# Performance work log

Hardware: AMD Instinct MI355X
Metric: run time of the kernel (lower is better)

Reference implementation:

```python
import jax, jax.numpy as jnp
import numpy as np

B, T, C, H = 8, 1024, 768, 12
D = C // H  # head_dim = 64


def setup_inputs() -> dict:
    key = jax.random.key(0)
    ks = jax.random.split(key, 5)
    return {
        "x": jax.random.normal(ks[0], (B, T, C), dtype=jnp.float32),
        "W_in": jax.random.normal(ks[1], (C, 3 * C), dtype=jnp.float32) * 0.02,
        "b_in": jax.random.normal(ks[2], (3 * C,), dtype=jnp.float32) * 0.02,
        "W_out": jax.random.normal(ks[3], (C, C), dtype=jnp.float32) * 0.02,
        "b_out": jax.random.normal(ks[4], (C,), dtype=jnp.float32) * 0.02,
    }


def reference(x, W_in, b_in, W_out, b_out):
    b, t, c = x.shape
    qkv = x @ W_in + b_in                       # [b, t, 3c]
    # NOTE: original code splits as (k, q, v) -- k first!
    k, q, v = jnp.split(qkv, 3, axis=2)
    # [b, h, t, d]
    k = k.reshape(b, t, H, D).transpose(0, 2, 1, 3)
    q = q.reshape(b, t, H, D).transpose(0, 2, 1, 3)
    v = v.reshape(b, t, H, D).transpose(0, 2, 1, 3)
    # NOTE: original applies NO 1/sqrt(d) scaling.
    scores = jnp.einsum("bhqd,bhkd->bhqk", q, k)
    causal = jnp.tril(jnp.ones((t, t), dtype=bool))
    scores = jnp.where(causal[None, None], scores, -jnp.inf)
    attn = jax.nn.softmax(scores, axis=-1)
    y = jnp.einsum("bhqk,bhkd->bhqd", attn, v)  # [b, h, t, d]
    y = y.transpose(0, 2, 1, 3).reshape(b, t, c)
    return y @ W_out + b_out
```

## Files before the change

kernel.cpp:

```cpp
#include <hip/hip_runtime.h>
#include <hip/hip_bf16.h>
#include <stdint.h>


typedef __bf16 bf16;
typedef __attribute__((ext_vector_type(4))) __bf16 bf16x4;
typedef __attribute__((ext_vector_type(8))) __bf16 bf16x8;
typedef __attribute__((ext_vector_type(4))) float f32x4;

#define NB 8
#define NT 1024
#define NC 768
#define NH 12
#define ND 64
#define NM (NB*NT)
#define N3C (3*NC)

typedef __attribute__((address_space(1))) void as1_void;
typedef __attribute__((address_space(3))) void as3_void;

__device__ __forceinline__ void gload_lds16(const void* g, void* l) {
  __builtin_amdgcn_global_load_lds((as1_void*)g, (as3_void*)l, 16, 0, 0);
}


__global__ void k_convert(const float* __restrict__ src, bf16* __restrict__ dst, int n4) {
  int i = blockIdx.x * blockDim.x + threadIdx.x;
  if (i < n4) {
    float4 v = reinterpret_cast<const float4*>(src)[i];
    bf16x4 o = { (bf16)v.x, (bf16)v.y, (bf16)v.z, (bf16)v.w };
    reinterpret_cast<bf16x4*>(dst)[i] = o;
  }
}

__global__ void k_transpose_w(const float* __restrict__ src, bf16* __restrict__ dst,
                              int R, int C) {
  __shared__ float tile[32][33];
  const int c0 = blockIdx.x * 32, r0 = blockIdx.y * 32;
  const int tx = threadIdx.x & 31, ty = threadIdx.x >> 5;
#pragma unroll
  for (int i = 0; i < 4; i++)
    tile[ty + i*8][tx] = src[(size_t)(r0 + ty + i*8) * C + c0 + tx];
  __syncthreads();
#pragma unroll
  for (int i = 0; i < 4; i++)
    dst[(size_t)(c0 + ty + i*8) * R + r0 + tx] = (bf16)tile[tx][ty + i*8];
}

template<int MODE, int TM>
__global__ void __launch_bounds__(256, (TM == 128 ? 3 : 4))
k_gemm_bt(const bf16* __restrict__ A, const bf16* __restrict__ Bt,
          const float* __restrict__ bias, float* __restrict__ Cout,
          bf16* __restrict__ qp, bf16* __restrict__ kp,
          bf16* __restrict__ vp,
          int M, int N, int K) {
  constexpr int ACH = TM / 64;
  constexpr int MF  = TM / 32;
  constexpr int WM  = TM / 2;
  __shared__ __align__(16) bf16 As[3][TM*32];
  __shared__ __align__(16) bf16 Bs[3][128*32];
  const int tm = blockIdx.x * TM, tn = blockIdx.y * 128;
  const int tid = threadIdx.x, lane = tid & 63, w = tid >> 6;
  const int wr = w >> 1, wc = w & 1;
  const int lr = lane & 15, lhi = lane >> 4;
  const int srow = tid >> 2;
  const int scol = ((tid & 3) ^ ((tid >> 3) & 3)) * 8;
  const int cswz = (lhi ^ ((lr >> 1) & 3)) * 16;
  const int nk = K / 32;

  auto stage = [&](bf16* as, bf16* bs, int kt) {
#pragma unroll
    for (int ch = 0; ch < ACH; ch++)
      gload_lds16(A + (size_t)(tm + ch*64 + srow) * K + kt + scol,
                  (char*)as + ch*4096 + tid*16);
#pragma unroll
    for (int ch = 0; ch < 2; ch++)
      gload_lds16(Bt + (size_t)(tn + ch*64 + srow) * K + kt + scol,
                  (char*)bs + ch*4096 + tid*16);
  };

  f32x4 acc[MF][4];
#pragma unroll
  for (int m = 0; m < MF; m++)
#pragma unroll
    for (int n = 0; n < 4; n++) acc[m][n] = (f32x4){0.f, 0.f, 0.f, 0.f};

  bf16 *a0 = As[0], *a1 = As[1], *a2 = As[2];
  bf16 *b0 = Bs[0], *b1 = Bs[1], *b2 = Bs[2];
  stage(a0, b0, 0);
  stage(a1, b1, 32);

  for (int t = 0; t < nk; ++t) {
    const int ktn = (t + 2 < nk ? t + 2 : nk - 1) * 32;
    stage(a2, b2, ktn);
    if constexpr (ACH == 2) asm volatile("s_waitcnt vmcnt(8)" ::: "memory");
    else                    asm volatile("s_waitcnt vmcnt(6)" ::: "memory");
    __builtin_amdgcn_s_barrier();

    bf16x8 af[MF], bfr[4];
#pragma unroll
    for (int m = 0; m < MF; m++)
      af[m] = *reinterpret_cast<const bf16x8*>(
          (const char*)a0 + (wr*WM + m*16 + lr) * 64 + cswz);
#pragma unroll
    for (int n = 0; n < 4; n++)
      bfr[n] = *reinterpret_cast<const bf16x8*>(
          (const char*)b0 + (wc*64 + n*16 + lr) * 64 + cswz);
#pragma unroll
    for (int m = 0; m < MF; m++)
#pragma unroll
      for (int n = 0; n < 4; n++)
        acc[m][n] = __builtin_amdgcn_mfma_f32_16x16x32_bf16(af[m], bfr[n], acc[m][n], 0, 0, 0);

    __builtin_amdgcn_s_barrier();

    bf16* ra = a0; a0 = a1; a1 = a2; a2 = ra;
    bf16* rb = b0; b0 = b1; b1 = b2; b2 = rb;
  }
  asm volatile("s_waitcnt vmcnt(0)" ::: "memory");

  if (MODE == 0) {
#pragma unroll
    for (int m = 0; m < MF; m++)
#pragma unroll
      for (int n = 0; n < 4; n++) {
        const int col = tn + wc*64 + n*16 + lr;
        const float bv = bias[col];
#pragma unroll
        for (int j = 0; j < 4; j++) {
          const int row = tm + wr*WM + m*16 + lhi*4 + j;
          Cout[(size_t)row * N + col] = acc[m][n][j] + bv;
        }
      }
  } else {
    const int part = tn / NC;
#pragma unroll
    for (int m = 0; m < MF; m++)
#pragma unroll
      for (int n = 0; n < 4; n++) {
        const int col = tn + wc*64 + n*16 + lr;
        const float bv = bias[col];
        const int cp = col - part * NC;
        const int h = cp >> 6, d = cp & 63;
#pragma unroll
        for (int j = 0; j < 4; j++) {
          const int row = tm + wr*WM + m*16 + lhi*4 + j;
          const int b0i = row >> 10, t = row & 1023;
          const int bh = b0i * NH + h;
          const bf16 val = (bf16)(acc[m][n][j] + bv);
          if (part == 2) {
            const size_t idx =
                ((((size_t)bh*16 + (t>>6))*4 + (d>>4))*2 + ((t>>5)&1))*512
                + (size_t)((d&15) + ((t>>3)&3)*16)*8 + (t&7);
            vp[idx] = val;
          } else {
            const size_t idx =
                (((size_t)bh*64 + (t>>4))*2 + (d>>5))*512
                + (size_t)(((d>>3)&3)*16 + (t&15))*8 + (d&7);
            if (part == 0) kp[idx] = val; else qp[idx] = val;
          }
        }
      }
  }
}

__global__ void __launch_bounds__(64, 2)
k_attn(const bf16* __restrict__ qpack, const bf16* __restrict__ kpack,
       const bf16* __restrict__ vpack, bf16* __restrict__ y) {
  const int bh = blockIdx.x, b = bh / NH, h = bh % NH;
  const int p = blockIdx.y;
  const int lane = threadIdx.x;
  const int lr = lane & 15, lhi = lane >> 4;
  __shared__ __align__(16) bf16 P[32][68];

#define LOAD_K(DST, K0)                                                        \
  {                                                                            \
    _Pragma("unroll")                                                          \
    for (int g = 0; g < 4; g++)                                                \
      _Pragma("unroll")                                                        \
      for (int h2 = 0; h2 < 2; h2++)                                           \
        DST[g][h2] = *reinterpret_cast<const bf16x8*>(                         \
            kpack + (((size_t)bh*64 + ((K0)>>4) + g)*2 + h2)*512 + lane*8);    \
  }

#define ATTN_STEP(KCUR, KNXT, KB)                                              \
  {                                                                            \
    const int k0 = (KB) * 64;                                                  \
    const int kn = ((KB) + 1 < nkb) ? k0 + 64 : k0;                            \
                        \
    bf16x8 vf[4][2];                                                           \
    _Pragma("unroll")                                                          \
    for (int dg = 0; dg < 4; dg++)                                             \
      _Pragma("unroll")                                                        \
      for (int kk = 0; kk < 2; kk++)                                           \
        vf[dg][kk] = *reinterpret_cast<const bf16x8*>(                         \
            vpack + ((((size_t)bh*16 + (k0>>6))*4 + dg)*2 + kk)*512 + lane*8); \
                   \
    LOAD_K(KNXT, kn);                                                          \
    f32x4 S[2][4];                                                             \
    _Pragma("unroll")                                                          \
    for (int m = 0; m < 2; m++)                                                \
      _Pragma("unroll")                                                        \
      for (int g = 0; g < 4; g++) S[m][g] = (f32x4){0.f, 0.f, 0.f, 0.f};       \
    _Pragma("unroll")                                                          \
    for (int g = 0; g < 4; g++)                                                \
      _Pragma("unroll")                                                        \
      for (int m = 0; m < 2; m++) {                                            \
        S[m][g] = __builtin_amdgcn_mfma_f32_16x16x32_bf16(qf[m][0], KCUR[g][0],\
                                                          S[m][g], 0, 0, 0);   \
        S[m][g] = __builtin_amdgcn_mfma_f32_16x16x32_bf16(qf[m][1], KCUR[g][1],\
                                                          S[m][g], 0, 0, 0);   \
      }                                                                        \
    const bool need_mask = ((KB) == nkb - 1);                                  \
    _Pragma("unroll")                                                          \
    for (int m = 0; m < 2; m++)                                                \
      _Pragma("unroll")                                                        \
      for (int g = 0; g < 4; g++) {                                            \
        const int key = k0 + g*16 + lr;                                        \
        _Pragma("unroll")                                                      \
        for (int j = 0; j < 4; j++) {                                          \
          float s = S[m][g][j];                                                \
          if (need_mask) {                                                     \
            const int row = qbase + m*16 + lhi*4 + j;                          \
            if (key > row) s = -1e30f;                                         \
          }                                                                    \
          const float ppv = __expf(s);   \
          L[m][j] += ppv;                                                      \
          P[m*16 + lhi*4 + j][g*16 + lr] = (bf16)ppv;                          \
        }                                                                      \
      }                                                                        \
    _Pragma("unroll")                                                          \
    for (int m = 0; m < 2; m++)                                                \
      _Pragma("unroll")                                                        \
      for (int kk = 0; kk < 2; kk++) {                                         \
        bf16x8 pf = *reinterpret_cast<const bf16x8*>(&P[m*16 + lr][kk*32 + lhi*8]); \
        _Pragma("unroll")                                                      \
        for (int dg = 0; dg < 4; dg++)                                         \
          O[m][dg] = __builtin_amdgcn_mfma_f32_16x16x32_bf16(pf, vf[dg][kk],   \
                                                             O[m][dg], 0, 0, 0); \
      }                                                                        \
  }

#pragma unroll 1
  for (int half = 0; half < 2; half++) {
    const int qt = half ? (31 - p) : p;
    const int qbase = qt * 32;
    const int nkb = (qbase >> 6) + 1;

    bf16x8 qf[2][2];
#pragma unroll
    for (int m = 0; m < 2; m++)
#pragma unroll
      for (int kk = 0; kk < 2; kk++)
        qf[m][kk] = *reinterpret_cast<const bf16x8*>(
            qpack + (((size_t)bh*64 + (qbase>>4) + m)*2 + kk)*512 + lane*8);

    f32x4 O[2][4];
    float L[2][4];
#pragma unroll
    for (int m = 0; m < 2; m++) {
#pragma unroll
      for (int d = 0; d < 4; d++) O[m][d] = (f32x4){0.f, 0.f, 0.f, 0.f};
#pragma unroll
      for (int j = 0; j < 4; j++) L[m][j] = 0.f;
    }

    bf16x8 kfA[4][2], kfB[4][2];
    LOAD_K(kfA, 0);
    int kb = 0;
#pragma unroll 1
    while (true) {
      ATTN_STEP(kfA, kfB, kb);
      kb++;
      if (kb >= nkb) break;
      ATTN_STEP(kfB, kfA, kb);
      kb++;
      if (kb >= nkb) break;
    }

#pragma unroll
    for (int m = 0; m < 2; m++)
#pragma unroll
      for (int j = 0; j < 4; j++) {
        float l = L[m][j];
        l += __shfl_xor(l, 1);
        l += __shfl_xor(l, 2);
        l += __shfl_xor(l, 4);
        l += __shfl_xor(l, 8);
        L[m][j] = 1.0f / l;
      }

#pragma unroll
    for (int m = 0; m < 2; m++)
#pragma unroll
      for (int dg = 0; dg < 4; dg++)
#pragma unroll
        for (int j = 0; j < 4; j++) {
          const int row = qbase + m*16 + lhi*4 + j;
          const int col = h*ND + dg*16 + lr;
          y[(size_t)(b*NT + row) * NC + col] = (bf16)(O[m][dg][j] * L[m][j]);
        }
  }
#undef ATTN_STEP
#undef LOAD_K
}

extern "C" void kernel_launch(void* const* d_in, const int* in_sizes, int n_in,
                              void* d_out, int out_size, void* d_ws, size_t ws_size,
                              hipStream_t stream) {
  const float* x     = (const float*)d_in[0];
  const float* W_in  = (const float*)d_in[1];
  const float* b_in  = (const float*)d_in[2];
  const float* W_out = (const float*)d_in[3];
  const float* b_out = (const float*)d_in[4];
  float* out = (float*)d_out;
  char* ws = (char*)d_ws;

  bf16* xb    = (bf16*)(ws + 0);
  bf16* Wit   = (bf16*)(ws + 12582912);
  bf16* Wot   = (bf16*)(ws + 16121856);
  bf16* qpack = (bf16*)(ws + 17301504);
  bf16* kpack = (bf16*)(ws + 29884416);
  bf16* vpack = (bf16*)(ws + 42467328);

  k_convert<<<6144, 256, 0, stream>>>(x, xb, NM * NC / 4);
  k_transpose_w<<<dim3(N3C/32, NC/32), 256, 0, stream>>>(W_in, Wit, NC, N3C);
  k_transpose_w<<<dim3(NC/32, NC/32), 256, 0, stream>>>(W_out, Wot, NC, NC);

  k_gemm_bt<1,128><<<dim3(NM/128, N3C/128), 256, 0, stream>>>(
      xb, Wit, b_in, nullptr, qpack, kpack, vpack, NM, N3C, NC);

  k_attn<<<dim3(NB*NH, 16), 64, 0, stream>>>(qpack, kpack, vpack, xb );

  k_gemm_bt<0,64><<<dim3(NM/64, NC/128), 256, 0, stream>>>(
      xb, Wot, b_out, out, nullptr, nullptr, nullptr, NM, NC, NC);
}
```

Before: 198.4 us.

## Switch GEMM to BK=64 double-buffered pipeline with XOR swizzle and grouped tile order

The GEMM k-loop now stages 64-wide K tiles into two LDS buffers instead of 32-wide tiles into three, so there are half as many barrier iterations. The LDS swizzle becomes an 8-way XOR over 128-byte rows. Blocks are remapped with a strided linear order to improve L2 locality. Launch-bounds occupancy hints are lowered to match the larger LDS footprint. Prefetch depth drops from two tiles to one, so less load latency may be hidden.

```diff
diff --git a/kernel.cpp b/kernel.cpp
--- a/kernel.cpp
+++ b/kernel.cpp
@@ -48,34 +48,40 @@
 }
 
 template<int MODE, int TM>
-__global__ void __launch_bounds__(256, (TM == 128 ? 3 : 4))
+__global__ void __launch_bounds__(256, (TM == 128 ? 2 : 3))
 k_gemm_bt(const bf16* __restrict__ A, const bf16* __restrict__ Bt,
           const float* __restrict__ bias, float* __restrict__ Cout,
           bf16* __restrict__ qp, bf16* __restrict__ kp,
           bf16* __restrict__ vp,
           int M, int N, int K) {
-  constexpr int ACH = TM / 64;
   constexpr int MF  = TM / 32;
   constexpr int WM  = TM / 2;
-  __shared__ __align__(16) bf16 As[3][TM*32];
-  __shared__ __align__(16) bf16 Bs[3][128*32];
-  const int tm = blockIdx.x * TM, tn = blockIdx.y * 128;
+  constexpr int NLD = MF + 4;
+  __shared__ __align__(16) bf16 As[2][TM*64];
+  __shared__ __align__(16) bf16 Bs[2][128*64];
+
+  const int gx = gridDim.x;
+  int lin = blockIdx.y * gx + blockIdx.x;
+  const int cpx = (gx * gridDim.y) >> 3;
+  lin = (lin & 7) * cpx + (lin >> 3);
+  const int tm = (lin % gx) * TM, tn = (lin / gx) * 128;
+
   const int tid = threadIdx.x, lane = tid & 63, w = tid >> 6;
   const int wr = w >> 1, wc = w & 1;
   const int lr = lane & 15, lhi = lane >> 4;
-  const int srow = tid >> 2;
-  const int scol = ((tid & 3) ^ ((tid >> 3) & 3)) * 8;
-  const int cswz = (lhi ^ ((lr >> 1) & 3)) * 16;
-  const int nk = K / 32;
+  const int rsw = lr & 7;
+  const int sr = tid >> 3;
+  const int sc = ((tid & 7) ^ (sr & 7)) * 8;
+  const int nk = K / 64;
 
   auto stage = [&](bf16* as, bf16* bs, int kt) {
 #pragma unroll
-    for (int ch = 0; ch < ACH; ch++)
-      gload_lds16(A + (size_t)(tm + ch*64 + srow) * K + kt + scol,
+    for (int ch = 0; ch < MF; ch++)
+      gload_lds16(A + (size_t)(tm + ch*32 + sr) * K + kt + sc,
                   (char*)as + ch*4096 + tid*16);
 #pragma unroll
-    for (int ch = 0; ch < 2; ch++)
-      gload_lds16(Bt + (size_t)(tn + ch*64 + srow) * K + kt + scol,
+    for (int ch = 0; ch < 4; ch++)
+      gload_lds16(Bt + (size_t)(tn + ch*32 + sr) * K + kt + sc,
                   (char*)bs + ch*4096 + tid*16);
   };
 
@@ -85,37 +91,39 @@
 #pragma unroll
     for (int n = 0; n < 4; n++) acc[m][n] = (f32x4){0.f, 0.f, 0.f, 0.f};
 
-  bf16 *a0 = As[0], *a1 = As[1], *a2 = As[2];
-  bf16 *b0 = Bs[0], *b1 = Bs[1], *b2 = Bs[2];
-  stage(a0, b0, 0);
-  stage(a1, b1, 32);
+  stage(As[0], Bs[0], 0);
+  int cur = 0;
 
   for (int t = 0; t < nk; ++t) {
-    const int ktn = (t + 2 < nk ? t + 2 : nk - 1) * 32;
-    stage(a2, b2, ktn);
-    if constexpr (ACH == 2) asm volatile("s_waitcnt vmcnt(8)" ::: "memory");
-    else                    asm volatile("s_waitcnt vmcnt(6)" ::: "memory");
+    const int ktn = (t + 1 < nk ? t + 1 : t) * 64;
+    stage(As[cur ^ 1], Bs[cur ^ 1], ktn);
+    asm volatile("s_waitcnt vmcnt(%0)" :: "i"(NLD) : "memory");
     __builtin_amdgcn_s_barrier();
 
-    bf16x8 af[MF], bfr[4];
-#pragma unroll
-    for (int m = 0; m < MF; m++)
-      af[m] = *reinterpret_cast<const bf16x8*>(
-          (const char*)a0 + (wr*WM + m*16 + lr) * 64 + cswz);
-#pragma unroll
-    for (int n = 0; n < 4; n++)
-      bfr[n] = *reinterpret_cast<const bf16x8*>(
-          (const char*)b0 + (wc*64 + n*16 + lr) * 64 + cswz);
-#pragma unroll
-    for (int m = 0; m < MF; m++)
+    const char* a0 = (const char*)As[cur];
+    const char* b0 = (const char*)Bs[cur];
+#pragma unroll
+    for (int kk = 0; kk < 2; kk++) {
+      bf16x8 af[MF], bfr[4];
+#pragma unroll
+      for (int m = 0; m < MF; m++)
+        af[m] = *reinterpret_cast<const bf16x8*>(
+            a0 + (wr*WM + m*16 + lr) * 128 + (((kk*4 + lhi) ^ rsw) << 4));
 #pragma unroll
       for (int n = 0; n < 4; n++)
-        acc[m][n] = __builtin_amdgcn_mfma_f32_16x16x32_bf16(af[m], bfr[n], acc[m][n], 0, 0, 0);
-
+        bfr[n] = *reinterpret_cast<const bf16x8*>(
+            b0 + (wc*64 + n*16 + lr) * 128 + (((kk*4 + lhi) ^ rsw) << 4));
+#pragma unroll
+      for (int m = 0; m < MF; m++)
+#pragma unroll
+        for (int n = 0; n < 4; n++)
+          acc[m][n] = __builtin_amdgcn_mfma_f32_16x16x32_bf16(af[m], bfr[n], acc[m][n], 0, 0, 0);
+    }
+
+    asm volatile("s_waitcnt lgkmcnt(0)" ::: "memory");
+    __builtin_amdgcn_sched_barrier(0);
     __builtin_amdgcn_s_barrier();
-
-    bf16* ra = a0; a0 = a1; a1 = a2; a2 = ra;
-    bf16* rb = b0; b0 = b1; b1 = b2; b2 = rb;
+    cur ^= 1;
   }
   asm volatile("s_waitcnt vmcnt(0)" ::: "memory");
 
```

After: 204.3 us. 2.9% more time.
